# Optimization experiments

Hardware: AMD Instinct MI355X
Metric: run time of the kernel (lower is better)

Reference implementation:

```python
import jax, jax.numpy as jnp
import numpy as np
from jax import lax

N, D, K = 8192, 1024, 80
M = 2048            # pre-NMS candidate budget (jit-static stand-in for nonzero())
TOPK = 100
IMG_H, IMG_W = 800.0, 1216.0
BW = (10.0, 10.0, 5.0, 5.0)            # Box2BoxTransform weights
SCALE_CLAMP = float(np.log(1000.0 / 16.0))
SCORE_T, NMS_T = 0.05, 0.5
MAX_COORD = max(IMG_H, IMG_W) + 1.0    # class offset for batched NMS


def setup_inputs() -> dict:
    key = jax.random.key(0)
    ks = jax.random.split(key, 5)
    x = jax.random.normal(ks[0], (N, D), jnp.float32)
    cls_w = jax.random.normal(ks[1], (D, K + 1), jnp.float32) * 0.1
    cls_b = jnp.zeros((K + 1,), jnp.float32)
    bbox_w = jax.random.normal(ks[2], (D, K * 4), jnp.float32) * 0.001
    bbox_b = jnp.zeros((K * 4,), jnp.float32)
    xy = jax.random.uniform(ks[3], (N, 2)) * jnp.array([IMG_W * 0.8, IMG_H * 0.8])
    wh = jax.random.uniform(ks[4], (N, 2)) * jnp.array([IMG_W * 0.2, IMG_H * 0.2]) + 8.0
    proposals = jnp.concatenate([xy, xy + wh], axis=1).astype(jnp.float32)  # [N,4] xyxy
    return {"x": x, "cls_w": cls_w, "cls_b": cls_b,
            "bbox_w": bbox_w, "bbox_b": bbox_b, "proposals": proposals}


def _apply_deltas(deltas, boxes):
    # deltas [N,K,4], boxes [N,4] xyxy -> decoded [N,K,4]
    w = boxes[:, 2] - boxes[:, 0]
    h = boxes[:, 3] - boxes[:, 1]
    cx = boxes[:, 0] + 0.5 * w
    cy = boxes[:, 1] + 0.5 * h
    dx = deltas[..., 0] / BW[0]
    dy = deltas[..., 1] / BW[1]
    dw = jnp.minimum(deltas[..., 2] / BW[2], SCALE_CLAMP)
    dh = jnp.minimum(deltas[..., 3] / BW[3], SCALE_CLAMP)
    pcx = dx * w[:, None] + cx[:, None]
    pcy = dy * h[:, None] + cy[:, None]
    pw = jnp.exp(dw) * w[:, None]
    ph = jnp.exp(dh) * h[:, None]
    return jnp.stack([pcx - 0.5 * pw, pcy - 0.5 * ph,
                      pcx + 0.5 * pw, pcy + 0.5 * ph], axis=-1)


def _clip(b):
    x1 = jnp.clip(b[..., 0], 0.0, IMG_W)
    y1 = jnp.clip(b[..., 1], 0.0, IMG_H)
    x2 = jnp.clip(b[..., 2], 0.0, IMG_W)
    y2 = jnp.clip(b[..., 3], 0.0, IMG_H)
    return jnp.stack([x1, y1, x2, y2], axis=-1)


def _pairwise_iou(b):  # [M,4] -> [M,M]
    x1 = jnp.maximum(b[:, None, 0], b[None, :, 0])
    y1 = jnp.maximum(b[:, None, 1], b[None, :, 1])
    x2 = jnp.minimum(b[:, None, 2], b[None, :, 2])
    y2 = jnp.minimum(b[:, None, 3], b[None, :, 3])
    inter = jnp.maximum(x2 - x1, 0.0) * jnp.maximum(y2 - y1, 0.0)
    area = (b[:, 2] - b[:, 0]) * (b[:, 3] - b[:, 1])
    union = area[:, None] + area[None, :] - inter
    return inter / jnp.maximum(union, 1e-9)


def _pipeline(x, cls_w, cls_b, bbox_w, bbox_b, proposals):
    probs = jax.nn.softmax(x @ cls_w + cls_b, axis=-1)[:, :K]   # drop bg col
    deltas = (x @ bbox_w + bbox_b).reshape(N, K, 4)
    boxes = _clip(_apply_deltas(deltas, proposals))             # [N,K,4]

    flat = probs.reshape(-1)                                    # [N*K]
    cand = jnp.where(flat > SCORE_T, flat, -1.0)
    top_scores, top_idx = lax.top_k(cand, M)                    # sorted desc
    prop_idx = top_idx // K
    cls_idx = top_idx % K
    cand_boxes = boxes[prop_idx, cls_idx]                       # [M,4]
    valid = top_scores > SCORE_T

    # batched NMS via per-class coordinate offsets
    off = cls_idx.astype(cand_boxes.dtype)[:, None] * MAX_COORD
    iou = _pairwise_iou(cand_boxes + off)
    idxs = jnp.arange(M)

    def body(i, sup):
        alive = jnp.logical_and(~sup[i], valid[i])
        return sup | (alive & (iou[i] > NMS_T) & (idxs > i))

    sup = lax.fori_loop(0, M, body, jnp.zeros((M,), bool))
    keep = valid & ~sup

    kept_scores = jnp.where(keep, top_scores, -1.0)
    fscores, fidx = lax.top_k(kept_scores, TOPK)
    fboxes = cand_boxes[fidx]
    fcls = cls_idx[fidx]
    fvalid = keep[fidx]
    return fboxes, fscores, fcls, fvalid


def reference(x, cls_w, cls_b, bbox_w, bbox_b, proposals):
    return _pipeline(x, cls_w, cls_b, bbox_w, bbox_b, proposals)
```

## Files before the change

kernel.cpp:

```cpp
#include <hip/hip_runtime.h>
#include <math.h>

typedef unsigned long long u64;
typedef unsigned int u32;

#define N_ROWS 8192
#define DIM 1024
#define KCLS 80
#define KC1 81
#define MCAND 2048
#define TOPK_ 100
#define CMAX 65536
#define ECAP 4096
#define ROWS_CAP 4096
#define EROWS 3
#define NSPLIT 16
#define NBINS 8192
#define BIN_BASE 125440
#define LCAP 1024
#define SCORE_T 0.05
#define NMS_T 0.5f
#define MAX_COORD_F 1217.0f
#define SCALE_CLAMP_F 4.135166556742356f
#define IMG_W_F 1216.0f
#define IMG_H_F 800.0f

#define GBM 32
#define GBK 64
#define PSTR 96
#define WFRAG (32 * 6 * 64 * 8)

typedef __attribute__((ext_vector_type(8))) short bf16x8;
typedef __attribute__((ext_vector_type(4))) float f32x4;

__device__ __forceinline__ int score_bin_f(float p) {
  u32 bits = __float_as_uint(p);
  int b = (int)(bits >> 13) - BIN_BASE;
  return b < 0 ? 0 : (b > NBINS - 1 ? NBINS - 1 : b);
}

__device__ __forceinline__ u64 readlane64(u64 v, int l) {
  u32 lo = __builtin_amdgcn_readlane((u32)v, l);
  u32 hi = __builtin_amdgcn_readlane((u32)(v >> 32), l);
  return ((u64)hi << 32) | (u64)lo;
}

__device__ __forceinline__ ushort f32_bf16(float f) {
  u32 b = __float_as_uint(f);
  b += 0x7FFFu + ((b >> 16) & 1u);
  return (ushort)(b >> 16);
}

__global__ __launch_bounds__(256) void k_prep(
    int* counter, int* ecount, int* rowcnt, int* hist, int* cnt,
    u32* rowflag, double* selS, u32* selI,
    const float4* __restrict__ bw4, float4* __restrict__ wT4,
    const float* __restrict__ w, ushort* __restrict__ whiF,
    ushort* __restrict__ wloF)
{
  int t = blockIdx.x * 256 + threadIdx.x;
  if (t == 0) { *counter = 0; *ecount = 0; *rowcnt = 0; }
  if (t < NBINS) hist[t] = 0;
  if (t < N_ROWS) rowflag[t] = 0;
  if (t < ECAP) cnt[t] = 0;
  if (t < MCAND) { selS[t] = -1.0; selI[t] = 0u; }
  if (t < KCLS * DIM) {
    int k = t / KCLS;
    int cls = t - k * KCLS;
    wT4[(size_t)cls * DIM + k] = bw4[t];
  }
  if (t < WFRAG) {
    int j = t & 7;
    int l = (t >> 3) & 63;
    int sf = t >> 9;
    int f = sf % 6;
    int s = sf / 6;
    int k = s * 32 + (l >> 4) * 8 + j;
    int c = f * 16 + (l & 15);
    float v = (c < KC1) ? w[(size_t)k * KC1 + c] : 0.0f;
    ushort hi = f32_bf16(v);
    float hf = __uint_as_float((u32)hi << 16);
    whiF[t] = hi;
    wloF[t] = f32_bf16(v - hf);
  }
}

__global__ __launch_bounds__(256) void k_gemm_sm(
    const float* __restrict__ x, const ushort* __restrict__ whiF,
    const ushort* __restrict__ wloF, const float* __restrict__ bias,
    float* __restrict__ scf, u32* __restrict__ cid,
    int* __restrict__ counter, int* __restrict__ hist)
{
  __shared__ __align__(16) char smem[33792];
  __shared__ float lgs[GBM * PSTR];
  __shared__ int lcnt, gbase;

  ushort (*xhi)[72] = (ushort(*)[72])(smem);
  ushort (*xlo)[72] = (ushort(*)[72])(smem + 4608);
  uint4* bhi = (uint4*)(smem + 9216);
  uint4* blo = (uint4*)(smem + 21504);
  u32* lhist = (u32*)(smem);
  float* lscf = (float*)(smem + 16384);
  u32* lcid = (u32*)(smem + 20480);
  float (*red)[32] = (float(*)[32])(smem + 24576);
  float* rowM = (float*)(smem + 26624);
  float* rowS = (float*)(smem + 26752);

  const int tid = threadIdx.x;
  const int rb = blockIdx.x * GBM;
  const int l = tid & 63;
  const int wv = tid >> 6;
  const int rh = wv & 1;
  const int ch = wv >> 1;

  if (tid == 0) lcnt = 0;

  f32x4 acc0 = {0.f, 0.f, 0.f, 0.f};
  f32x4 acc1 = {0.f, 0.f, 0.f, 0.f};
  f32x4 acc2 = {0.f, 0.f, 0.f, 0.f};

  const int srow = tid >> 3;
  const int skq = (tid & 7) * 8;
  const float* xsrc = x + (size_t)(rb + srow) * DIM + skq;

  const int ar = rh * 16 + (l & 15);
  const int ak = (l >> 4) * 8;
  const int bbase = (ch * 3) * 64 + l;

  for (int kt = 0; kt < DIM; kt += GBK) {
    float4 xv0 = *(const float4*)(xsrc + kt);
    float4 xv1 = *(const float4*)(xsrc + kt + 4);
    const uint4* bh = (const uint4*)whiF + (size_t)(kt >> 5) * 384;
    const uint4* bl = (const uint4*)wloF + (size_t)(kt >> 5) * 384;
    uint4 h0 = bh[tid], h1 = bh[tid + 256], h2 = bh[tid + 512];
    uint4 g0 = bl[tid], g1 = bl[tid + 256], g2 = bl[tid + 512];

    __syncthreads();

    {
      float vv[8] = {xv0.x, xv0.y, xv0.z, xv0.w, xv1.x, xv1.y, xv1.z, xv1.w};
      u32 hw[4], lw[4];
#pragma unroll
      for (int q = 0; q < 4; ++q) {
        ushort ha = f32_bf16(vv[2 * q]);
        ushort hb = f32_bf16(vv[2 * q + 1]);
        ushort la = f32_bf16(vv[2 * q] - __uint_as_float((u32)ha << 16));
        ushort lb = f32_bf16(vv[2 * q + 1] - __uint_as_float((u32)hb << 16));
        hw[q] = (u32)ha | ((u32)hb << 16);
        lw[q] = (u32)la | ((u32)lb << 16);
      }
      *(uint4*)&xhi[srow][skq] = make_uint4(hw[0], hw[1], hw[2], hw[3]);
      *(uint4*)&xlo[srow][skq] = make_uint4(lw[0], lw[1], lw[2], lw[3]);
      bhi[tid] = h0; bhi[tid + 256] = h1; bhi[tid + 512] = h2;
      blo[tid] = g0; blo[tid + 256] = g1; blo[tid + 512] = g2;
    }
    __syncthreads();

#pragma unroll
    for (int ks = 0; ks < 2; ++ks) {
      bf16x8 ah = *(const bf16x8*)&xhi[ar][ks * 32 + ak];
      bf16x8 al = *(const bf16x8*)&xlo[ar][ks * 32 + ak];
      bf16x8 b0h = *(const bf16x8*)&bhi[ks * 384 + bbase];
      bf16x8 b0l = *(const bf16x8*)&blo[ks * 384 + bbase];
      bf16x8 b1h = *(const bf16x8*)&bhi[ks * 384 + bbase + 64];
      bf16x8 b1l = *(const bf16x8*)&blo[ks * 384 + bbase + 64];
      bf16x8 b2h = *(const bf16x8*)&bhi[ks * 384 + bbase + 128];
      bf16x8 b2l = *(const bf16x8*)&blo[ks * 384 + bbase + 128];
      acc0 = __builtin_amdgcn_mfma_f32_16x16x32_bf16(ah, b0h, acc0, 0, 0, 0);
      acc0 = __builtin_amdgcn_mfma_f32_16x16x32_bf16(ah, b0l, acc0, 0, 0, 0);
      acc0 = __builtin_amdgcn_mfma_f32_16x16x32_bf16(al, b0h, acc0, 0, 0, 0);
      acc1 = __builtin_amdgcn_mfma_f32_16x16x32_bf16(ah, b1h, acc1, 0, 0, 0);
      acc1 = __builtin_amdgcn_mfma_f32_16x16x32_bf16(ah, b1l, acc1, 0, 0, 0);
      acc1 = __builtin_amdgcn_mfma_f32_16x16x32_bf16(al, b1h, acc1, 0, 0, 0);
      acc2 = __builtin_amdgcn_mfma_f32_16x16x32_bf16(ah, b2h, acc2, 0, 0, 0);
      acc2 = __builtin_amdgcn_mfma_f32_16x16x32_bf16(ah, b2l, acc2, 0, 0, 0);
      acc2 = __builtin_amdgcn_mfma_f32_16x16x32_bf16(al, b2h, acc2, 0, 0, 0);
    }
  }

  __syncthreads();
  {
    const int row0l = rh * 16 + (l >> 4) * 4;
    const int col0 = ch * 48 + (l & 15);
#pragma unroll
    for (int r = 0; r < 4; ++r) {
      lgs[(row0l + r) * PSTR + col0 + 0]  = acc0[r];
      lgs[(row0l + r) * PSTR + col0 + 16] = acc1[r];
      lgs[(row0l + r) * PSTR + col0 + 32] = acc2[r];
    }
  }
  for (int e = tid; e < NBINS / 2; e += 256) lhist[e] = 0u;
  __syncthreads();

  const int cx = tid >> 4;
  const int ry = tid & 15;
  float lg[2][6];
#pragma unroll
  for (int i = 0; i < 2; i++) {
    int rloc = ry * 2 + i;
#pragma unroll
    for (int j = 0; j < 6; j++) {
      int c = cx * 6 + j;
      lg[i][j] = (c < KC1) ? (lgs[rloc * PSTR + c] + bias[c]) : -1e30f;
    }
  }
  float pm[2] = {-1e30f, -1e30f};
#pragma unroll
  for (int i = 0; i < 2; i++)
#pragma unroll
    for (int j = 0; j < 6; j++) pm[i] = fmaxf(pm[i], lg[i][j]);
  red[cx][ry * 2 + 0] = pm[0];
  red[cx][ry * 2 + 1] = pm[1];
  __syncthreads();
  if (tid < 32) {
    float m = -1e30f;
#pragma unroll
    for (int q = 0; q < 16; q++) m = fmaxf(m, red[q][tid]);
    rowM[tid] = m;
  }
  __syncthreads();
  float ps[2] = {0.0f, 0.0f};
#pragma unroll
  for (int i = 0; i < 2; i++) {
    float m = rowM[ry * 2 + i];
#pragma unroll
    for (int j = 0; j < 6; j++) {
      int c = cx * 6 + j;
      if (c < KC1) ps[i] += expf(lg[i][j] - m);
    }
  }
  __syncthreads();
  red[cx][ry * 2 + 0] = ps[0];
  red[cx][ry * 2 + 1] = ps[1];
  __syncthreads();
  if (tid < 32) {
    float s = 0.0f;
#pragma unroll
    for (int q = 0; q < 16; q++) s += red[q][tid];
    rowS[tid] = s;
  }
  __syncthreads();
#pragma unroll
  for (int i = 0; i < 2; i++) {
    int rloc = ry * 2 + i;
    float m = rowM[rloc], s = rowS[rloc];
#pragma unroll
    for (int j = 0; j < 6; j++) {
      int c = cx * 6 + j;
      if (c < KCLS) {
        float p = expf(lg[i][j] - m) / s;
        if (p > 0.0485f) {
          int pos = atomicAdd(&lcnt, 1);
          u32 idx = (u32)((rb + rloc) * KCLS + c);
          if (pos < LCAP) { lscf[pos] = p; lcid[pos] = idx; }
          else {
            int g = atomicAdd(counter, 1);
            if (g < CMAX) { scf[g] = p; cid[g] = idx; }
          }
        }
        if (p > 0.051f) {
          int b = score_bin_f(p);
          atomicAdd(&lhist[b >> 1], 1u << ((b & 1) * 16));
        }
      }
    }
  }
  __syncthreads();
  if (tid == 0) {
    int n = min(lcnt, LCAP);
    gbase = atomicAdd(counter, n);
  }
  __syncthreads();
  {
    int n = min(lcnt, LCAP);
    for (int e = tid; e < n; e += 256) {
      int g = gbase + e;
      if (g < CMAX) { scf[g] = lscf[e]; cid[g] = lcid[e]; }
    }
  }
  for (int q = tid; q < NBINS / 2; q += 256) {
    u32 v = lhist[q];
    if (v) {
      u32 lo = v & 0xFFFFu, hi = v >> 16;
      if (lo) atomicAdd(&hist[q * 2 + 0], (int)lo);
      if (hi) atomicAdd(&hist[q * 2 + 1], (int)hi);
    }
  }
}

__global__ __launch_bounds__(256) void k_superset(
    const float* __restrict__ scf, const u32* __restrict__ cid,
    const int* __restrict__ counter, const int* __restrict__ hist,
    u32* __restrict__ elist, int* __restrict__ ecount, u32* __restrict__ rowflag)
{
  __shared__ int h[NBINS];
  __shared__ int segsum[256];
  __shared__ int segsuf[256];
  __shared__ int tbin_s;
  int C = *counter; if (C > CMAX) C = CMAX;
  if (blockIdx.x * 256 >= C) return;
  const int tid = threadIdx.x;
  if (tid == 0) tbin_s = 0;
  for (int e = tid; e < NBINS; e += 256) h[e] = hist[e];
  __syncthreads();
  {
    int s = 0;
#pragma unroll
    for (int q = 0; q < NBINS / 256; ++q) s += h[tid * (NBINS / 256) + q];
    segsum[tid] = s;
  }
  __syncthreads();
  if (tid == 0) {
    int run = 0;
    for (int t = 255; t >= 0; --t) { segsuf[t] = run; run += segsum[t]; }
  }
  __syncthreads();
  {
    int run = segsuf[tid];
    if (run < MCAND) {
      const int lo = tid * (NBINS / 256);
      for (int b = lo + NBINS / 256 - 1; b >= lo; --b) {
        run += h[b];
        if (run >= MCAND) { tbin_s = b; break; }
      }
    }
  }
  __syncthreads();
  int TM = tbin_s - 6; if (TM < 0) TM = 0;
  int e = blockIdx.x * 256 + tid;
  const int lane = tid & 63;
  bool pred = false;
  if (e < C) pred = (score_bin_f(scf[e]) >= TM);
  u64 m = __ballot(pred);
  if (m) {
    int leader = __ffsll((long long)m) - 1;
    int base = 0;
    if (lane == leader) base = atomicAdd(ecount, (int)__popcll(m));
    base = __shfl(base, leader);
    if (pred) {
      int j = base + (int)__popcll(m & ((lane == 63) ? ~0ull >> 1 : ((1ull << lane) - 1)));
      if (j < ECAP) {
        u32 idx = cid[e];
        elist[j] = idx;
        rowflag[idx / KCLS] = 1u;
      }
    }
  }
}

__global__ __launch_bounds__(256) void k_rowlist(
    const u32* __restrict__ rowflag, int* __restrict__ rowslot,
    u32* __restrict__ rowlist, int* __restrict__ rowcnt)
{
  int r = blockIdx.x * 256 + threadIdx.x;
  const int lane = threadIdx.x & 63;
  bool pred = (r < N_ROWS) && rowflag[r];
  u64 m = __ballot(pred);
  if (m) {
    int leader = __ffsll((long long)m) - 1;
    int base = 0;
    if (lane == leader) base = atomicAdd(rowcnt, (int)__popcll(m));
    base = __shfl(base, leader);
    if (pred) {
      int s = base + (int)__popcll(m & ((lane == 63) ? ~0ull >> 1 : ((1ull << lane) - 1)));
      if (s < ROWS_CAP) { rowslot[r] = s; rowlist[s] = (u32)r; }
    }
  }
}

__global__ __launch_bounds__(256) void k_exact(
    const u32* __restrict__ rowlist, const int* __restrict__ rowcnt,
    const float* __restrict__ x, const float* __restrict__ w,
    const float* __restrict__ bias, double* __restrict__ prow)
{
  __shared__ double xt[EROWS][DIM];
  __shared__ double red[EROWS][128];
  int rc = *rowcnt; if (rc > ROWS_CAP) rc = ROWS_CAP;
  const int rb = blockIdx.x * EROWS;
  if (rb >= rc) return;
  const int tid = threadIdx.x;

  for (int q = tid; q < EROWS * (DIM / 4); q += 256) {
    int srow = q >> 8;
    int sf = q & 255;
    int slot = rb + srow; if (slot >= rc) slot = rb;
    const float* xrow = x + (size_t)rowlist[slot] * DIM;
    float4 xv = *(const float4*)(xrow + sf * 4);
    xt[srow][sf * 4 + 0] = (double)xv.x;
    xt[srow][sf * 4 + 1] = (double)xv.y;
    xt[srow][sf * 4 + 2] = (double)xv.z;
    xt[srow][sf * 4 + 3] = (double)xv.w;
  }
  for (int q = tid; q < EROWS * 128; q += 256) ((double*)red)[q] = -1e300;
  __syncthreads();

  const int row = tid / KC1;
  const int c = tid - row * KC1;
  const bool act = (row < EROWS);
  double a = 0.0;
  if (act) {
    const double* xr = xt[row];
    double a0 = 0.0, a1 = 0.0, a2 = 0.0, a3 = 0.0;
#pragma unroll 8
    for (int kk = 0; kk < DIM / 4; ++kk) {
      a0 = fma(xr[kk          ], (double)w[(size_t)(kk          ) * KC1 + c], a0);
      a1 = fma(xr[kk + 256    ], (double)w[(size_t)(kk + 256    ) * KC1 + c], a1);
      a2 = fma(xr[kk + 512    ], (double)w[(size_t)(kk + 512    ) * KC1 + c], a2);
      a3 = fma(xr[kk + 768    ], (double)w[(size_t)(kk + 768    ) * KC1 + c], a3);
    }
    a = a0 + a1 + a2 + a3 + (double)bias[c];
    red[row][c] = a;
  }
  __syncthreads();
  if (act && c < 64) { double o = red[row][c + 64]; if (o > red[row][c]) red[row][c] = o; }
  __syncthreads();
#pragma unroll
  for (int off = 32; off > 0; off >>= 1) {
    if (act && c < off) { double o = red[row][c + off]; if (o > red[row][c]) red[row][c] = o; }
    __syncthreads();
  }
  double m = act ? red[row][0] : 0.0;
  __syncthreads();
  double e = act ? exp(a - m) : 0.0;
  for (int q = tid; q < EROWS * 128; q += 256) ((double*)red)[q] = 0.0;
  __syncthreads();
  if (act) red[row][c] = e;
  __syncthreads();
  if (act && c < 64) red[row][c] += red[row][c + 64];
  __syncthreads();
#pragma unroll
  for (int off = 32; off > 0; off >>= 1) {
    if (act && c < off) red[row][c] += red[row][c + off];
    __syncthreads();
  }
  if (act && rb + row < rc) {
    double s = red[row][0];
    prow[(size_t)(rb + row) * KC1 + c] = e / s;
  }
}

__global__ __launch_bounds__(256) void k_build(
    const u32* __restrict__ elist, const int* __restrict__ ecount,
    const int* __restrict__ rowslot, const double* __restrict__ prow,
    double* __restrict__ ssc, u32* __restrict__ sid)
{
  int E = *ecount; if (E > ECAP) E = ECAP;
  int e = blockIdx.x * 256 + threadIdx.x;
  if (e < E) {
    u32 idx = elist[e];
    int row = (int)(idx / KCLS);
    int cls = (int)(idx - (u32)row * KCLS);
    double p = prow[(size_t)rowslot[row] * KC1 + cls];
    ssc[e] = (p > SCORE_T) ? p : -1.0;
    sid[e] = idx;
  }
}

__global__ __launch_bounds__(256) void k_rank(
    const double* __restrict__ ssc, const u32* __restrict__ sid,
    const int* __restrict__ ecount, int* __restrict__ cnt)
{
  __shared__ double lsc[512];
  __shared__ u32 lid[512];
  int S = *ecount; if (S > ECAP) S = ECAP;
  const int i = blockIdx.x * 256 + threadIdx.x;
  if (blockIdx.x * 256 >= S) return;
  const double si = (i < S) ? ssc[i] : -2.0;
  const u32 ii = (i < S) ? sid[i] : 0u;
  const int seg = (S + NSPLIT - 1) / NSPLIT;
  const int jlo = blockIdx.y * seg;
  const int jhi = min(S, jlo + seg);
  int c = 0;
  for (int base = jlo; base < jhi; base += 512) {
    const int n = min(512, jhi - base);
    __syncthreads();
    for (int e = threadIdx.x; e < n; e += 256) { lsc[e] = ssc[base + e]; lid[e] = sid[base + e]; }
    __syncthreads();
    if (i < S) {
      int j = 0;
      for (; j + 8 <= n; j += 8) {
        double s0 = lsc[j + 0], s1 = lsc[j + 1], s2 = lsc[j + 2], s3 = lsc[j + 3];
        double s4 = lsc[j + 4], s5 = lsc[j + 5], s6 = lsc[j + 6], s7 = lsc[j + 7];
        u32 d0 = lid[j + 0], d1 = lid[j + 1], d2 = lid[j + 2], d3 = lid[j + 3];
        u32 d4 = lid[j + 4], d5 = lid[j + 5], d6 = lid[j + 6], d7 = lid[j + 7];
        c += (s0 > si || (s0 == si && d0 < ii)) ? 1 : 0;
        c += (s1 > si || (s1 == si && d1 < ii)) ? 1 : 0;
        c += (s2 > si || (s2 == si && d2 < ii)) ? 1 : 0;
        c += (s3 > si || (s3 == si && d3 < ii)) ? 1 : 0;
        c += (s4 > si || (s4 == si && d4 < ii)) ? 1 : 0;
        c += (s5 > si || (s5 == si && d5 < ii)) ? 1 : 0;
        c += (s6 > si || (s6 == si && d6 < ii)) ? 1 : 0;
        c += (s7 > si || (s7 == si && d7 < ii)) ? 1 : 0;
      }
      for (; j < n; ++j) {
        double sj = lsc[j];
        c += (sj > si || (sj == si && lid[j] < ii)) ? 1 : 0;
      }
    }
  }
  if (i < S && c > 0) atomicAdd(&cnt[i], c);
}

__global__ __launch_bounds__(256) void k_scatter(
    const double* __restrict__ ssc, const u32* __restrict__ sid,
    const int* __restrict__ ecount, const int* __restrict__ cnt,
    double* __restrict__ selS, u32* __restrict__ selI)
{
  int S = *ecount; if (S > ECAP) S = ECAP;
  const int i = blockIdx.x * 256 + threadIdx.x;
  if (i < S) {
    int c = cnt[i];
    if (c < MCAND) { selS[c] = ssc[i]; selI[c] = sid[i]; }
  }
}

__global__ __launch_bounds__(256) void k_gather_decode(
    const double* __restrict__ selS, const u32* __restrict__ selI,
    const float* __restrict__ x, const float4* __restrict__ wT4,
    const float* __restrict__ bbias, const float* __restrict__ proposals,
    float4* __restrict__ dbox, float4* __restrict__ obox,
    float* __restrict__ areav, float* __restrict__ scorev,
    int* __restrict__ clsv, int* __restrict__ validv)
{
  __shared__ double wred[4][4];
  const int r = blockIdx.x;
  const double s = selS[r];
  const u32 idx = selI[r];
  const int row = (int)(idx / 80u);
  const int cls = (int)(idx - (u32)row * 80u);

  const float* xr = x + (size_t)row * DIM;
  const float4* wc = wT4 + (size_t)cls * DIM;
  double a0 = 0, a1 = 0, a2 = 0, a3 = 0;
  for (int k = threadIdx.x; k < DIM; k += 256) {
    double xv = (double)xr[k];
    float4 wv = wc[k];
    a0 = fma(xv, (double)wv.x, a0);
    a1 = fma(xv, (double)wv.y, a1);
    a2 = fma(xv, (double)wv.z, a2);
    a3 = fma(xv, (double)wv.w, a3);
  }
#pragma unroll
  for (int off = 32; off > 0; off >>= 1) {
    a0 += __shfl_down(a0, off);
    a1 += __shfl_down(a1, off);
    a2 += __shfl_down(a2, off);
    a3 += __shfl_down(a3, off);
  }
  int lane = threadIdx.x & 63, wid = threadIdx.x >> 6;
  if (lane == 0) { wred[wid][0] = a0; wred[wid][1] = a1; wred[wid][2] = a2; wred[wid][3] = a3; }
  __syncthreads();
  if (threadIdx.x == 0) {
    double d0 = wred[0][0] + wred[1][0] + wred[2][0] + wred[3][0] + (double)bbias[cls * 4 + 0];
    double d1 = wred[0][1] + wred[1][1] + wred[2][1] + wred[3][1] + (double)bbias[cls * 4 + 1];
    double d2 = wred[0][2] + wred[1][2] + wred[2][2] + wred[3][2] + (double)bbias[cls * 4 + 2];
    double d3 = wred[0][3] + wred[1][3] + wred[2][3] + wred[3][3] + (double)bbias[cls * 4 + 3];
    float4 p = ((const float4*)proposals)[row];
    float w = p.z - p.x, h = p.w - p.y;
    float cxx = p.x + 0.5f * w, cyy = p.y + 0.5f * h;
    float dx = (float)d0 / 10.0f;
    float dy = (float)d1 / 10.0f;
    float dw = fminf((float)d2 / 5.0f, SCALE_CLAMP_F);
    float dh = fminf((float)d3 / 5.0f, SCALE_CLAMP_F);
    float pcx = dx * w + cxx, pcy = dy * h + cyy;
    float pw = expf(dw) * w, ph = expf(dh) * h;
    float x1 = pcx - 0.5f * pw, y1 = pcy - 0.5f * ph;
    float x2 = pcx + 0.5f * pw, y2 = pcy + 0.5f * ph;
    x1 = fminf(fmaxf(x1, 0.0f), IMG_W_F);
    x2 = fminf(fmaxf(x2, 0.0f), IMG_W_F);
    y1 = fminf(fmaxf(y1, 0.0f), IMG_H_F);
    y2 = fminf(fmaxf(y2, 0.0f), IMG_H_F);
    float4 db = {x1, y1, x2, y2};
    dbox[r] = db;
    float ofs = (float)cls * MAX_COORD_F;
    float4 ob = {x1 + ofs, y1 + ofs, x2 + ofs, y2 + ofs};
    obox[r] = ob;
    areav[r] = (ob.z - ob.x) * (ob.w - ob.y);
    scorev[r] = (float)s;
    clsv[r] = cls;
    validv[r] = (s > SCORE_T) ? 1 : 0;
  }
}

__global__ __launch_bounds__(256) void k_nms_mask(
    const float4* __restrict__ obox, const float* __restrict__ areav,
    u64* __restrict__ maskT)
{
  __shared__ float4 sb[MCAND];
  __shared__ float sa[MCAND];
  const int i = blockIdx.x;
  for (int e = threadIdx.x; e < MCAND; e += 256) { sb[e] = obox[e]; sa[e] = areav[e]; }
  __syncthreads();
  float4 bi = sb[i];
  float ai = sa[i];
  int lane = threadIdx.x & 63, wid = threadIdx.x >> 6;
#pragma unroll
  for (int it = 0; it < MCAND / 256; ++it) {
    int j = it * 256 + threadIdx.x;
    float4 bj = sb[j];
    float xx1 = fmaxf(bi.x, bj.x);
    float yy1 = fmaxf(bi.y, bj.y);
    float xx2 = fminf(bi.z, bj.z);
    float yy2 = fminf(bi.w, bj.w);
    float inter = fmaxf(xx2 - xx1, 0.0f) * fmaxf(yy2 - yy1, 0.0f);
    float uni = ai + sa[j] - inter;
    float iou = inter / fmaxf(uni, 1e-9f);
    bool pred = (iou > NMS_T) && (j > i);
    u64 b = __ballot(pred);
    if (lane == 0) maskT[(size_t)(it * 4 + wid) * MCAND + i] = b;
  }
}

__global__ __launch_bounds__(256) void k_nms_fin(
    const u64* __restrict__ maskT, const int* __restrict__ validv,
    const float4* __restrict__ dbox, const float* __restrict__ scorev,
    const int* __restrict__ clsv, float* __restrict__ out)
{
  __shared__ int vsh[MCAND];
  __shared__ char ksh[MCAND];
  __shared__ short fidx[TOPK_];
  const int tid = threadIdx.x;

  for (int e = tid; e < MCAND; e += 256) vsh[e] = validv[e];
  __syncthreads();

  if (tid < 64) {
    const int lane = tid;
    u64 validw = 0;
    for (int k = 0; k < 32; ++k) {
      u64 b = __ballot(vsh[k * 64 + lane] != 0);
      validw = (lane == k) ? b : validw;
    }

    u64 alivew = 0;
    u64 supw = 0;
    int total = 0;
    int lastc = 31;

    for (int c = 0; c < 32; ++c) {
      const u64* col = maskT + (size_t)c * MCAND;
      u64 acc = 0;
      for (int t0 = 0; t0 < c; t0 += 8) {
        u64 r0 = 0, r1 = 0, r2 = 0, r3 = 0, r4 = 0, r5 = 0, r6 = 0, r7 = 0;
        if (t0 + 0 < c) r0 = col[(t0 + 0) * 64 + lane];
        if (t0 + 1 < c) r1 = col[(t0 + 1) * 64 + lane];
        if (t0 + 2 < c) r2 = col[(t0 + 2) * 64 + lane];
        if (t0 + 3 < c) r3 = col[(t0 + 3) * 64 + lane];
        if (t0 + 4 < c) r4 = col[(t0 + 4) * 64 + lane];
        if (t0 + 5 < c) r5 = col[(t0 + 5) * 64 + lane];
        if (t0 + 6 < c) r6 = col[(t0 + 6) * 64 + lane];
        if (t0 + 7 < c) r7 = col[(t0 + 7) * 64 + lane];
        u64 a;
        a = readlane64(alivew, t0 + 0); acc |= r0 & ((u64)0 - ((a >> lane) & 1ull));
        if (t0 + 1 < c) { a = readlane64(alivew, t0 + 1); acc |= r1 & ((u64)0 - ((a >> lane) & 1ull)); }
        if (t0 + 2 < c) { a = readlane64(alivew, t0 + 2); acc |= r2 & ((u64)0 - ((a >> lane) & 1ull)); }
        if (t0 + 3 < c) { a = readlane64(alivew, t0 + 3); acc |= r3 & ((u64)0 - ((a >> lane) & 1ull)); }
        if (t0 + 4 < c) { a = readlane64(alivew, t0 + 4); acc |= r4 & ((u64)0 - ((a >> lane) & 1ull)); }
        if (t0 + 5 < c) { a = readlane64(alivew, t0 + 5); acc |= r5 & ((u64)0 - ((a >> lane) & 1ull)); }
        if (t0 + 6 < c) { a = readlane64(alivew, t0 + 6); acc |= r6 & ((u64)0 - ((a >> lane) & 1ull)); }
        if (t0 + 7 < c) { a = readlane64(alivew, t0 + 7); acc |= r7 & ((u64)0 - ((a >> lane) & 1ull)); }
      }
      u64 d = col[(size_t)c * 64 + lane];
      acc |= (u64)__shfl_xor((long long)acc, 1);
      acc |= (u64)__shfl_xor((long long)acc, 2);
      acc |= (u64)__shfl_xor((long long)acc, 4);
      acc |= (u64)__shfl_xor((long long)acc, 8);
      acc |= (u64)__shfl_xor((long long)acc, 16);
      acc |= (u64)__shfl_xor((long long)acc, 32);
      u64 s_sup = acc;
      u64 s_val = readlane64(validw, c);
      u64 aliveM = 0;
#pragma unroll
      for (int b = 0; b < 64; ++b) {
        u32 rhi = __builtin_amdgcn_readlane((u32)(d >> 32), b);
        u32 rlo = (b < 31) ? __builtin_amdgcn_readlane((u32)d, b) : 0u;
        u64 row = ((u64)rhi << 32) | (u64)rlo;
        u64 act = ((s_val >> b) & 1ull) & (~(s_sup >> b) & 1ull);
        s_sup |= row & ((u64)0 - act);
        aliveM |= act << b;
      }
      alivew = (lane == c) ? aliveM : alivew;
      supw   = (lane == c) ? s_sup  : supw;
      total += (int)__popcll(aliveM);
      if (total >= TOPK_) { lastc = c; break; }
    }

    for (int k = 0; k < 32; ++k) {
      int e = k * 64 + lane;
      if (k <= lastc) {
        u64 s = readlane64(supw, k);
        int sb = (int)((s >> lane) & 1ull);
        ksh[e] = (char)((vsh[e] && !sb) ? 1 : 0);
      } else {
        ksh[e] = 0;
      }
    }
  }
  __syncthreads();
  if (tid == 0) {
    int cnt = 0;
    for (int r = 0; r < MCAND && cnt < TOPK_; ++r) if (ksh[r]) fidx[cnt++] = (short)r;
    for (int r = 0; r < MCAND && cnt < TOPK_; ++r) if (!ksh[r]) fidx[cnt++] = (short)r;
  }
  __syncthreads();
  if (tid < TOPK_) {
    int r = fidx[tid];
    float4 b = dbox[r];
    out[tid * 4 + 0] = b.x; out[tid * 4 + 1] = b.y;
    out[tid * 4 + 2] = b.z; out[tid * 4 + 3] = b.w;
    int kp = ksh[r];
    out[400 + tid] = kp ? scorev[r] : -1.0f;
    out[500 + tid] = (float)clsv[r];
    out[600 + tid] = kp ? 1.0f : 0.0f;
  }
}

extern "C" void kernel_launch(void* const* d_in, const int* in_sizes, int n_in,
                              void* d_out, int out_size, void* d_ws, size_t ws_size,
                              hipStream_t stream) {
  const float* x         = (const float*)d_in[0];
  const float* cls_w     = (const float*)d_in[1];
  const float* cls_b     = (const float*)d_in[2];
  const float* bbox_w    = (const float*)d_in[3];
  const float* bbox_b    = (const float*)d_in[4];
  const float* proposals = (const float*)d_in[5];
  float* out = (float*)d_out;

  char* ws = (char*)d_ws;
  size_t off = 0;
  float4* wT4   = (float4*)(ws + off); off += (size_t)KCLS * DIM * 16;
  ushort* whiF  = (ushort*)(ws + off); off += (size_t)WFRAG * 2;
  ushort* wloF  = (ushort*)(ws + off); off += (size_t)WFRAG * 2;
  float*  scf   = (float*)(ws + off);  off += (size_t)CMAX * 4;
  u32*    cid   = (u32*)(ws + off);    off += (size_t)CMAX * 4;
  int*    hist  = (int*)(ws + off);    off += (size_t)NBINS * 4;
  u32*    rowflag = (u32*)(ws + off);  off += (size_t)N_ROWS * 4;
  int*    rowslot = (int*)(ws + off);  off += (size_t)N_ROWS * 4;
  u32*    rowlist = (u32*)(ws + off);  off += (size_t)ROWS_CAP * 4;
  u32*    elist = (u32*)(ws + off);    off += (size_t)ECAP * 4;
  double* prow  = (double*)(ws + off); off += (size_t)ROWS_CAP * KC1 * 8;
  double* ssc   = (double*)(ws + off); off += (size_t)ECAP * 8;
  u32*    sid   = (u32*)(ws + off);    off += (size_t)ECAP * 4;
  int*    cnt   = (int*)(ws + off);    off += (size_t)ECAP * 4;
  double* selS  = (double*)(ws + off); off += (size_t)MCAND * 8;
  u32*    selI  = (u32*)(ws + off);    off += (size_t)MCAND * 4;
  off = (off + 15) & ~(size_t)15;
  int*    counter = (int*)(ws + off);  off += 16;
  int*    ecount  = (int*)(ws + off);  off += 16;
  int*    rowcnt  = (int*)(ws + off);  off += 16;
  float4* dbox  = (float4*)(ws + off); off += (size_t)MCAND * 16;
  float4* obox  = (float4*)(ws + off); off += (size_t)MCAND * 16;
  float*  areav = (float*)(ws + off);  off += (size_t)MCAND * 4;
  float*  scorev= (float*)(ws + off);  off += (size_t)MCAND * 4;
  int*    clsv  = (int*)(ws + off);    off += (size_t)MCAND * 4;
  int*    validv= (int*)(ws + off);    off += (size_t)MCAND * 4;
  off = (off + 15) & ~(size_t)15;
  u64*    maskT = (u64*)(ws + off);    off += (size_t)MCAND * 32 * 8;

  k_prep<<<WFRAG / 256, 256, 0, stream>>>(counter, ecount, rowcnt, hist, cnt,
                                          rowflag, selS, selI,
                                          (const float4*)bbox_w, wT4,
                                          cls_w, whiF, wloF);
  k_gemm_sm<<<N_ROWS / GBM, 256, 0, stream>>>(x, whiF, wloF, cls_b,
                                              scf, cid, counter, hist);
  k_superset<<<CMAX / 256, 256, 0, stream>>>(scf, cid, counter, hist,
                                             elist, ecount, rowflag);
  k_rowlist<<<N_ROWS / 256, 256, 0, stream>>>(rowflag, rowslot, rowlist, rowcnt);
  k_exact<<<(ROWS_CAP + EROWS - 1) / EROWS, 256, 0, stream>>>(
      rowlist, rowcnt, x, cls_w, cls_b, prow);
  k_build<<<ECAP / 256, 256, 0, stream>>>(elist, ecount, rowslot, prow, ssc, sid);
  k_rank<<<dim3(ECAP / 256, NSPLIT), 256, 0, stream>>>(ssc, sid, ecount, cnt);
  k_scatter<<<ECAP / 256, 256, 0, stream>>>(ssc, sid, ecount, cnt, selS, selI);
  k_gather_decode<<<MCAND, 256, 0, stream>>>(selS, selI, x, wT4, bbox_b, proposals,
                                             dbox, obox, areav, scorev, clsv, validv);
  k_nms_mask<<<MCAND, 256, 0, stream>>>(obox, areav, maskT);
  k_nms_fin<<<1, 256, 0, stream>>>(maskT, validv, dbox, scorev, clsv, out);
}
```

Baseline: 215.6 us.

## Split exact fp64 softmax GEMM over K with transposed weights and partial sums

Splits the fp64 recompute of class logits for flagged rows into four K-slices, each its own block in a 2D grid. The partials go to a workspace and a second kernel sums them, adds bias and applies the softmax. The class weights are transposed in the prep kernel so each thread reads its column contiguously as float4, instead of strided scalar loads. This gives more parallelism and smaller shared memory per block, at the cost of an extra launch, a partial-sum buffer round trip, and a slightly different fp64 summation order.

```diff
diff --git a/kernel.cpp b/kernel.cpp
--- a/kernel.cpp
+++ b/kernel.cpp
@@ -14,6 +14,8 @@
 #define ECAP 4096
 #define ROWS_CAP 4096
 #define EROWS 3
+#define EKS 4
+#define EKL 256
 #define NSPLIT 16
 #define NBINS 8192
 #define BIN_BASE 125440
@@ -56,7 +58,7 @@
     u32* rowflag, double* selS, u32* selI,
     const float4* __restrict__ bw4, float4* __restrict__ wT4,
     const float* __restrict__ w, ushort* __restrict__ whiF,
-    ushort* __restrict__ wloF)
+    ushort* __restrict__ wloF, float* __restrict__ wcT)
 {
   int t = blockIdx.x * 256 + threadIdx.x;
   if (t == 0) { *counter = 0; *ecount = 0; *rowcnt = 0; }
@@ -68,6 +70,11 @@
     int k = t / KCLS;
     int cls = t - k * KCLS;
     wT4[(size_t)cls * DIM + k] = bw4[t];
+  }
+  if (t < KC1 * DIM) {
+    int c = t >> 10;
+    int k = t & 1023;
+    wcT[t] = w[(size_t)k * KC1 + c];
   }
   if (t < WFRAG) {
     int j = t & 7;
@@ -368,47 +375,74 @@
   }
 }
 
-__global__ __launch_bounds__(256) void k_exact(
+__global__ __launch_bounds__(256) void k_exact_part(
     const u32* __restrict__ rowlist, const int* __restrict__ rowcnt,
-    const float* __restrict__ x, const float* __restrict__ w,
+    const float* __restrict__ x, const float* __restrict__ wcT,
+    double* __restrict__ pexa)
+{
+  __shared__ double xt[EROWS][EKL];
+  int rc = *rowcnt; if (rc > ROWS_CAP) rc = ROWS_CAP;
+  const int rb = blockIdx.x * EROWS;
+  if (rb >= rc) return;
+  const int ks = blockIdx.y;
+  const int kt0 = ks * EKL;
+  const int tid = threadIdx.x;
+
+  if (tid < EROWS * (EKL / 4)) {
+    int srow = tid >> 6;
+    int sf = tid & 63;
+    int slot = rb + srow; if (slot >= rc) slot = rb;
+    const float* xrow = x + (size_t)rowlist[slot] * DIM + kt0;
+    float4 xv = *(const float4*)(xrow + sf * 4);
+    xt[srow][sf * 4 + 0] = (double)xv.x;
+    xt[srow][sf * 4 + 1] = (double)xv.y;
+    xt[srow][sf * 4 + 2] = (double)xv.z;
+    xt[srow][sf * 4 + 3] = (double)xv.w;
+  }
+  __syncthreads();
+
+  const int row = tid / KC1;
+  const int c = tid - row * KC1;
+  if (row < EROWS && rb + row < rc) {
+    const float4* wp = (const float4*)(wcT + (size_t)c * DIM + kt0);
+    const double* xr = xt[row];
+    double a = 0.0;
+#pragma unroll 8
+    for (int q = 0; q < EKL / 4; ++q) {
+      float4 wv = wp[q];
+      a = fma(xr[4 * q + 0], (double)wv.x, a);
+      a = fma(xr[4 * q + 1], (double)wv.y, a);
+      a = fma(xr[4 * q + 2], (double)wv.z, a);
+      a = fma(xr[4 * q + 3], (double)wv.w, a);
+    }
+    pexa[((size_t)(rb + row) * EKS + ks) * KC1 + c] = a;
+  }
+}
+
+__global__ __launch_bounds__(256) void k_exact_fin(
+    const double* __restrict__ pexa, const int* __restrict__ rowcnt,
     const float* __restrict__ bias, double* __restrict__ prow)
 {
-  __shared__ double xt[EROWS][DIM];
   __shared__ double red[EROWS][128];
   int rc = *rowcnt; if (rc > ROWS_CAP) rc = ROWS_CAP;
   const int rb = blockIdx.x * EROWS;
   if (rb >= rc) return;
   const int tid = threadIdx.x;
 
-  for (int q = tid; q < EROWS * (DIM / 4); q += 256) {
-    int srow = q >> 8;
-    int sf = q & 255;
-    int slot = rb + srow; if (slot >= rc) slot = rb;
-    const float* xrow = x + (size_t)rowlist[slot] * DIM;
-    float4 xv = *(const float4*)(xrow + sf * 4);
-    xt[srow][sf * 4 + 0] = (double)xv.x;
-    xt[srow][sf * 4 + 1] = (double)xv.y;
-    xt[srow][sf * 4 + 2] = (double)xv.z;
-    xt[srow][sf * 4 + 3] = (double)xv.w;
-  }
   for (int q = tid; q < EROWS * 128; q += 256) ((double*)red)[q] = -1e300;
   __syncthreads();
 
   const int row = tid / KC1;
   const int c = tid - row * KC1;
-  const bool act = (row < EROWS);
+  const bool act = (row < EROWS) && (rb + row < rc);
   double a = 0.0;
   if (act) {
-    const double* xr = xt[row];
-    double a0 = 0.0, a1 = 0.0, a2 = 0.0, a3 = 0.0;
-#pragma unroll 8
-    for (int kk = 0; kk < DIM / 4; ++kk) {
-      a0 = fma(xr[kk          ], (double)w[(size_t)(kk          ) * KC1 + c], a0);
-      a1 = fma(xr[kk + 256    ], (double)w[(size_t)(kk + 256    ) * KC1 + c], a1);
-      a2 = fma(xr[kk + 512    ], (double)w[(size_t)(kk + 512    ) * KC1 + c], a2);
-      a3 = fma(xr[kk + 768    ], (double)w[(size_t)(kk + 768    ) * KC1 + c], a3);
-    }
-    a = a0 + a1 + a2 + a3 + (double)bias[c];
+    const double* pp = pexa + ((size_t)(rb + row) * EKS) * KC1 + c;
+    a = pp[0 * KC1];
+    a += pp[1 * KC1];
+    a += pp[2 * KC1];
+    a += pp[3 * KC1];
+    a += (double)bias[c];
     red[row][c] = a;
   }
   __syncthreads();
@@ -433,7 +467,7 @@
     if (act && c < off) red[row][c] += red[row][c + off];
     __syncthreads();
   }
-  if (act && rb + row < rc) {
+  if (act) {
     double s = red[row][0];
     prow[(size_t)(rb + row) * KC1 + c] = e / s;
   }
@@ -729,8 +763,10 @@
   char* ws = (char*)d_ws;
   size_t off = 0;
   float4* wT4   = (float4*)(ws + off); off += (size_t)KCLS * DIM * 16;
+  float*  wcT   = (float*)(ws + off);  off += (size_t)KC1 * DIM * 4;
   ushort* whiF  = (ushort*)(ws + off); off += (size_t)WFRAG * 2;
   ushort* wloF  = (ushort*)(ws + off); off += (size_t)WFRAG * 2;
+  double* pexa  = (double*)(ws + off); off += (size_t)ROWS_CAP * EKS * KC1 * 8;
   float*  scf   = (float*)(ws + off);  off += (size_t)CMAX * 4;
   u32*    cid   = (u32*)(ws + off);    off += (size_t)CMAX * 4;
   int*    hist  = (int*)(ws + off);    off += (size_t)NBINS * 4;
@@ -760,14 +796,16 @@
   k_prep<<<WFRAG / 256, 256, 0, stream>>>(counter, ecount, rowcnt, hist, cnt,
                                           rowflag, selS, selI,
                                           (const float4*)bbox_w, wT4,
-                                          cls_w, whiF, wloF);
+                                          cls_w, whiF, wloF, wcT);
   k_gemm_sm<<<N_ROWS / GBM, 256, 0, stream>>>(x, whiF, wloF, cls_b,
                                               scf, cid, counter, hist);
   k_superset<<<CMAX / 256, 256, 0, stream>>>(scf, cid, counter, hist,
                                              elist, ecount, rowflag);
   k_rowlist<<<N_ROWS / 256, 256, 0, stream>>>(rowflag, rowslot, rowlist, rowcnt);
-  k_exact<<<(ROWS_CAP + EROWS - 1) / EROWS, 256, 0, stream>>>(
-      rowlist, rowcnt, x, cls_w, cls_b, prow);
+  k_exact_part<<<dim3((ROWS_CAP + EROWS - 1) / EROWS, EKS), 256, 0, stream>>>(
+      rowlist, rowcnt, x, wcT, pexa);
+  k_exact_fin<<<(ROWS_CAP + EROWS - 1) / EROWS, 256, 0, stream>>>(
+      pexa, rowcnt, cls_b, prow);
   k_build<<<ECAP / 256, 256, 0, stream>>>(elist, ecount, rowslot, prow, ssc, sid);
   k_rank<<<dim3(ECAP / 256, NSPLIT), 256, 0, stream>>>(ssc, sid, ecount, cnt);
   k_scatter<<<ECAP / 256, 256, 0, stream>>>(ssc, sid, ecount, cnt, selS, selI);
```

After: 254.2 us. +17.9%, slower.
